# Performance work log

Hardware: AMD Instinct MI355X
Metric: run time of the kernel (lower is better)

## Reference

```python
import jax, jax.numpy as jnp
import numpy as np

B, L, K, T, C_IN, C_OUT, TKS = 32, 1855, 7, 40, 8, 32, 5


def setup_inputs() -> dict:
    key = jax.random.key(0)
    k1, k2, k3, k4 = jax.random.split(key, 4)
    x = jax.random.normal(k1, (B, L, T, C_IN), dtype=jnp.float32)
    idx = jax.random.randint(k2, (L, K), 0, L, dtype=jnp.int32)
    missing = jax.random.uniform(k3, (L, K)) < 0.1
    neighbor_indices = jnp.where(missing, jnp.int32(-1), idx)
    fan_in = K * TKS * C_IN
    fan_out = K * TKS * C_OUT
    limit = np.sqrt(6.0 / (fan_in + fan_out))  # glorot uniform
    kernel = jax.random.uniform(k4, (K, TKS, C_IN, C_OUT), dtype=jnp.float32,
                                minval=-limit, maxval=limit)
    bias = jnp.zeros((C_OUT,), dtype=jnp.float32)
    return {"x": x, "neighbor_indices": neighbor_indices, "kernel": kernel, "bias": bias}


def reference(x, neighbor_indices, kernel, bias):
    # x: (B, L, T, C_in); neighbor_indices: (L, K) with -1 = missing
    mask = (neighbor_indices != -1)
    safe_idx = jnp.where(mask, neighbor_indices, 0)
    # gather neighbor features: (B, L, K, T, C_in)
    nf = x[:, safe_idx]
    nf = nf * mask[None, :, :, None, None].astype(x.dtype)
    tks = kernel.shape[1]
    t_out = x.shape[2] - tks + 1
    # valid temporal conv: sum over small fixed tau instead of materializing
    # the (B, L, K, T_out, tks, C_in) framed tensor
    out = jnp.zeros((x.shape[0], x.shape[1], t_out, kernel.shape[-1]), dtype=x.dtype)
    for tau in range(tks):
        out = out + jnp.einsum('blkti,kio->blto',
                               nf[:, :, :, tau:tau + t_out, :], kernel[:, tau])
    return out + bias
```

## Files before the change

kernel.cpp:

```cpp
#include <hip/hip_runtime.h>

constexpr int Bn = 32, Ln = 1855, Kn = 7, Tn = 40, CIn = 8, COn = 32, TKSn = 5, TOn = 36;
constexpr int BG   = 8;
constexpr int KRED = Kn * TKSn * CIn;
constexpr int KPAD = 288;
constexpr int WROW = 296;
constexpr int XS_ELEMS = BG * Kn * Tn * CIn;
constexpr int XS2 = 4 * Kn * Tn * CIn;
constexpr size_t XN = (size_t)Bn * Ln * Tn * CIn;

constexpr size_t WS_WT   = 0;
constexpr size_t WS_ZPAD = 18432;
constexpr size_t WS_XBF  = 18560;
constexpr size_t WS_NEED = WS_XBF + XN * 2;

typedef __attribute__((ext_vector_type(8))) short bf16x8;
typedef __attribute__((ext_vector_type(8))) unsigned short u16x8;
typedef __attribute__((ext_vector_type(4))) float f32x4;

__device__ inline unsigned short f2bf(float f) {
    unsigned u = __builtin_bit_cast(unsigned, f);
    u += 0x7fffu + ((u >> 16) & 1u);
    return (unsigned short)(u >> 16);
}

__device__ inline void gload_lds16(const void* g, void* lds) {
    __builtin_amdgcn_global_load_lds(
        (const __attribute__((address_space(1))) unsigned int*)g,
        (__attribute__((address_space(3))) unsigned int*)lds,
        16, 0, 0);
}


__global__ __launch_bounds__(256) void prep_w(const float* __restrict__ w,
                                              unsigned short* __restrict__ wt,
                                              unsigned short* __restrict__ zpad) {
    const int tid = threadIdx.x;
    for (int p = tid; p < KRED * COn; p += 256) {
        int o  = p & 31;
        int kr = p >> 5;
        wt[o * KPAD + kr] = f2bf(w[p]);
    }
    for (int p = tid; p < COn * (KPAD - KRED); p += 256) {
        int o = p >> 3;
        wt[o * KPAD + KRED + (p & 7)] = 0;
    }
    if (tid < 64) zpad[tid] = 0;
}

__global__ __launch_bounds__(256) void prep_x(const float* __restrict__ x,
                                              unsigned short* __restrict__ xbf) {
    const size_t n8 = XN / 8;
    for (size_t p = (size_t)blockIdx.x * 256 + threadIdx.x; p < n8;
         p += (size_t)gridDim.x * 256) {
        float4 a = ((const float4*)x)[2 * p];
        float4 b = ((const float4*)x)[2 * p + 1];
        u16x8 v;
        v[0] = f2bf(a.x); v[1] = f2bf(a.y); v[2] = f2bf(a.z); v[3] = f2bf(a.w);
        v[4] = f2bf(b.x); v[5] = f2bf(b.y); v[6] = f2bf(b.z); v[7] = f2bf(b.w);
        *(u16x8*)&xbf[p * 8] = v;
    }
}

__global__ __launch_bounds__(64, 2) void conv_mfma4(
    const unsigned short* __restrict__ xbf,
    const int*   __restrict__ nbr,
    const unsigned short* __restrict__ wt,
    const unsigned short* __restrict__ zpad,
    const float* __restrict__ bias,
    float*       __restrict__ out)
{
    __shared__ unsigned short xs[XS2 + 8];

    const int lane = threadIdx.x;
    const int l    = blockIdx.x;
    const int half = blockIdx.y & 1;
    const int bg   = blockIdx.y >> 1;
    const int b0   = bg * BG + half * 4;

    if (lane < 8) xs[XS2 + lane] = 0;

    int nv = 0;
    if (lane < Kn) nv = nbr[l * Kn + lane];

    #pragma unroll
    for (int s = 0; s < 18; ++s) {
        if (s < 17 || lane < 32) {
            const int u   = s * 64 + lane;
            const int row = u / 40;
            const int q   = u - row * 40;
            const int bl  = row / 7;
            const int k   = row - bl * 7;
            const int l2  = __shfl(nv, k);
            const unsigned short* src = zpad;
            if (l2 >= 0)
                src = xbf + ((size_t)(b0 + bl) * Ln + l2) * 320 + q * 8;
            gload_lds16(src, &xs[s * 512]);
        }
    }

    const int quad = lane >> 4;
    const int lrow = lane & 15;

    bf16x8 bfrag[2][9];
    #pragma unroll
    for (int oh = 0; oh < 2; ++oh)
        #pragma unroll
        for (int c = 0; c < 9; ++c)
            bfrag[oh][c] = *(const bf16x8*)(wt + (oh * 16 + lrow) * KPAD + c * 32 + quad * 8);
    const float bv0 = bias[lrow];
    const float bv1 = bias[16 + lrow];

    asm volatile("s_waitcnt vmcnt(0)" ::: "memory");

    #pragma unroll
    for (int g = 0; g < 3; ++g) {
        const int rt0 = g * 3;
        f32x4 a00 = {0.f,0.f,0.f,0.f};
        f32x4 acc00 = a00, acc01 = a00, acc10 = a00, acc11 = a00, acc20 = a00, acc21 = a00;
        const int m0 = (rt0 + 0) * 16 + lrow;
        const int m1 = (rt0 + 1) * 16 + lrow;
        const int m2 = (rt0 + 2) * 16 + lrow;
        const int bl0 = m0 / 36, t0 = m0 - bl0 * 36;
        const int bl1 = m1 / 36, t1 = m1 - bl1 * 36;
        const int bl2 = m2 / 36, t2 = m2 - bl2 * 36;
        const int base0 = bl0 * 2240 + t0 * 8;
        const int base1 = bl1 * 2240 + t1 * 8;
        const int base2 = bl2 * 2240 + t2 * 8;
        __builtin_amdgcn_s_setprio(1);
        #pragma unroll
        for (int c = 0; c < 9; ++c) {
            const int p = c * 4 + quad;
            const int knbr = p / 5, tau = p - knbr * 5;
            const int koff = knbr * 320 + tau * 8;
            int o0 = base0 + koff, o1 = base1 + koff, o2 = base2 + koff;
            if (c == 8 && quad == 3) { o0 = XS2; o1 = XS2; o2 = XS2; }
            bf16x8 a0 = *(const bf16x8*)&xs[o0];
            bf16x8 a1 = *(const bf16x8*)&xs[o1];
            bf16x8 a2 = *(const bf16x8*)&xs[o2];
            acc00 = __builtin_amdgcn_mfma_f32_16x16x32_bf16(a0, bfrag[0][c], acc00, 0, 0, 0);
            acc01 = __builtin_amdgcn_mfma_f32_16x16x32_bf16(a0, bfrag[1][c], acc01, 0, 0, 0);
            acc10 = __builtin_amdgcn_mfma_f32_16x16x32_bf16(a1, bfrag[0][c], acc10, 0, 0, 0);
            acc11 = __builtin_amdgcn_mfma_f32_16x16x32_bf16(a1, bfrag[1][c], acc11, 0, 0, 0);
            acc20 = __builtin_amdgcn_mfma_f32_16x16x32_bf16(a2, bfrag[0][c], acc20, 0, 0, 0);
            acc21 = __builtin_amdgcn_mfma_f32_16x16x32_bf16(a2, bfrag[1][c], acc21, 0, 0, 0);
        }
        __builtin_amdgcn_s_setprio(0);
        #pragma unroll
        for (int i = 0; i < 3; ++i) {
            const f32x4 c0 = (i == 0) ? acc00 : ((i == 1) ? acc10 : acc20);
            const f32x4 c1 = (i == 0) ? acc01 : ((i == 1) ? acc11 : acc21);
            const int rt = rt0 + i;
            #pragma unroll
            for (int reg = 0; reg < 4; ++reg) {
                const int m  = rt * 16 + quad * 4 + reg;
                const int bl = m / 36, t = m - bl * 36;
                const size_t off =
                    (((size_t)(b0 + bl) * Ln + l) * TOn + t) * COn + lrow;
                __builtin_nontemporal_store(c0[reg] + bv0, &out[off]);
                __builtin_nontemporal_store(c1[reg] + bv1, &out[off + 16]);
            }
        }
    }
}

__global__ __launch_bounds__(256) void conv_mfma(
    const float* __restrict__ x, const int* __restrict__ nbr,
    const float* __restrict__ w, const float* __restrict__ bias,
    float* __restrict__ out)
{
    __shared__ unsigned short xs[XS_ELEMS + 8];
    __shared__ unsigned short wt[COn * WROW];

    const int tid = threadIdx.x;
    const int l   = blockIdx.x;
    const int bg  = blockIdx.y;

    for (int p = tid; p < KRED * COn; p += 256) {
        int o  = p & 31;
        int kr = p >> 5;
        wt[o * WROW + kr] = f2bf(w[p]);
    }
    for (int p = tid; p < COn * (WROW - KRED); p += 256) {
        int o = p >> 4;
        wt[o * WROW + KRED + (p & 15)] = 0;
    }
    if (tid < 8) xs[XS_ELEMS + tid] = 0;

    for (int p = tid; p < BG * Kn * 80; p += 256) {
        int b_local = p / 560;
        int r = p - b_local * 560;
        int k = r / 80;
        int q = r - k * 80;
        int l2 = nbr[l * Kn + k];
        float4 v = make_float4(0.f, 0.f, 0.f, 0.f);
        if (l2 >= 0)
            v = ((const float4*)x)[((size_t)(bg * BG + b_local) * Ln + l2) * 80 + q];
        ushort4 pk;
        pk.x = f2bf(v.x); pk.y = f2bf(v.y); pk.z = f2bf(v.z); pk.w = f2bf(v.w);
        *(ushort4*)&xs[p * 4] = pk;
    }
    __syncthreads();

    const int wave = tid >> 6;
    const int lane = tid & 63;
    const int quad = lane >> 4;
    const int lrow = lane & 15;
    const int o_base  = (wave & 1) * 16;
    const int rt_base = (wave >> 1) * 9;

    bf16x8 bfrag[9];
    #pragma unroll
    for (int c = 0; c < 9; ++c)
        bfrag[c] = *(const bf16x8*)&wt[(o_base + lrow) * WROW + c * 32 + quad * 8];

    const float bv = bias[o_base + lrow];

    #pragma unroll
    for (int g = 0; g < 3; ++g) {
        const int rt0 = rt_base + g * 3;
        f32x4 acc0 = {0.f,0.f,0.f,0.f}, acc1 = acc0, acc2 = acc0;
        const int m0 = (rt0 + 0) * 16 + lrow;
        const int m1 = (rt0 + 1) * 16 + lrow;
        const int m2 = (rt0 + 2) * 16 + lrow;
        const int bl0 = m0 / 36, t0 = m0 - bl0 * 36;
        const int bl1 = m1 / 36, t1 = m1 - bl1 * 36;
        const int bl2 = m2 / 36, t2 = m2 - bl2 * 36;
        const int base0 = bl0 * 2240 + t0 * 8;
        const int base1 = bl1 * 2240 + t1 * 8;
        const int base2 = bl2 * 2240 + t2 * 8;
        #pragma unroll
        for (int c = 0; c < 9; ++c) {
            const int p = c * 4 + quad;
            const int knbr = p / 5, tau = p - knbr * 5;
            const int koff = knbr * 320 + tau * 8;
            int o0 = base0 + koff, o1 = base1 + koff, o2 = base2 + koff;
            if (c == 8 && quad == 3) { o0 = XS_ELEMS; o1 = XS_ELEMS; o2 = XS_ELEMS; }
            bf16x8 a0 = *(const bf16x8*)&xs[o0];
            bf16x8 a1 = *(const bf16x8*)&xs[o1];
            bf16x8 a2 = *(const bf16x8*)&xs[o2];
            acc0 = __builtin_amdgcn_mfma_f32_16x16x32_bf16(a0, bfrag[c], acc0, 0, 0, 0);
            acc1 = __builtin_amdgcn_mfma_f32_16x16x32_bf16(a1, bfrag[c], acc1, 0, 0, 0);
            acc2 = __builtin_amdgcn_mfma_f32_16x16x32_bf16(a2, bfrag[c], acc2, 0, 0, 0);
        }
        #pragma unroll
        for (int i = 0; i < 3; ++i) {
            const f32x4 acc = (i == 0) ? acc0 : ((i == 1) ? acc1 : acc2);
            const int rt = rt0 + i;
            #pragma unroll
            for (int reg = 0; reg < 4; ++reg) {
                const int m  = rt * 16 + quad * 4 + reg;
                const int bl = m / 36, t = m - bl * 36;
                const size_t off =
                    (((size_t)(bg * BG + bl) * Ln + l) * TOn + t) * COn + o_base + lrow;
                out[off] = acc[reg] + bv;
            }
        }
    }
}

extern "C" void kernel_launch(void* const* d_in, const int* in_sizes, int n_in,
                              void* d_out, int out_size, void* d_ws, size_t ws_size,
                              hipStream_t stream) {
    const float* x    = (const float*)d_in[0];
    const int*   nbr  = (const int*)d_in[1];
    const float* w    = (const float*)d_in[2];
    const float* bias = (const float*)d_in[3];
    float*       out  = (float*)d_out;

    if (ws_size >= WS_NEED && d_ws != nullptr) {
        unsigned short* wt   = (unsigned short*)((char*)d_ws + WS_WT);
        unsigned short* zpad = (unsigned short*)((char*)d_ws + WS_ZPAD);
        unsigned short* xbf  = (unsigned short*)((char*)d_ws + WS_XBF);
        prep_w<<<1, 256, 0, stream>>>(w, wt, zpad);
        prep_x<<<2048, 256, 0, stream>>>(x, xbf);
        conv_mfma4<<<dim3(Ln, 8), dim3(64), 0, stream>>>(xbf, nbr, wt, zpad, bias, out);
    } else {
        conv_mfma<<<dim3(Ln, Bn / BG), dim3(256), 0, stream>>>(x, nbr, w, bias, out);
    }
}
```

Baseline: 369.6 us.

## Merge prep kernels and split conv tiles across two waves per block

Folds the weight-prep and x-to-bf16 conversion kernels into a single launch, with one extra block dedicated to weights, which removes one kernel launch. The conv kernel goes from one 64-thread wave per block to two waves that split the gather of the 18 LDS chunks. The two waves then divide the 9 M-tiles 5/4 after a __syncthreads, with launch bounds changed to 128 threads and 4 blocks per CU. The aim is to shorten each block's serial gather and compute path and raise wave-level parallelism, at the cost of a block barrier and an uneven tile split.

```diff
diff --git a/kernel.cpp b/kernel.cpp
--- a/kernel.cpp
+++ b/kernel.cpp
@@ -31,28 +31,27 @@
         16, 0, 0);
 }
 
-
-__global__ __launch_bounds__(256) void prep_w(const float* __restrict__ w,
-                                              unsigned short* __restrict__ wt,
-                                              unsigned short* __restrict__ zpad) {
+__global__ __launch_bounds__(256) void prep_all(const float* __restrict__ x,
+                                                unsigned short* __restrict__ xbf,
+                                                const float* __restrict__ w,
+                                                unsigned short* __restrict__ wt,
+                                                unsigned short* __restrict__ zpad) {
     const int tid = threadIdx.x;
-    for (int p = tid; p < KRED * COn; p += 256) {
-        int o  = p & 31;
-        int kr = p >> 5;
-        wt[o * KPAD + kr] = f2bf(w[p]);
-    }
-    for (int p = tid; p < COn * (KPAD - KRED); p += 256) {
-        int o = p >> 3;
-        wt[o * KPAD + KRED + (p & 7)] = 0;
-    }
-    if (tid < 64) zpad[tid] = 0;
-}
-
-__global__ __launch_bounds__(256) void prep_x(const float* __restrict__ x,
-                                              unsigned short* __restrict__ xbf) {
+    if (blockIdx.x == 2048) {
+        for (int p = tid; p < KRED * COn; p += 256) {
+            int o  = p & 31;
+            int kr = p >> 5;
+            wt[o * KPAD + kr] = f2bf(w[p]);
+        }
+        for (int p = tid; p < COn * (KPAD - KRED); p += 256) {
+            int o = p >> 3;
+            wt[o * KPAD + KRED + (p & 7)] = 0;
+        }
+        if (tid < 64) zpad[tid] = 0;
+        return;
+    }
     const size_t n8 = XN / 8;
-    for (size_t p = (size_t)blockIdx.x * 256 + threadIdx.x; p < n8;
-         p += (size_t)gridDim.x * 256) {
+    for (size_t p = (size_t)blockIdx.x * 256 + tid; p < n8; p += (size_t)2048 * 256) {
         float4 a = ((const float4*)x)[2 * p];
         float4 b = ((const float4*)x)[2 * p + 1];
         u16x8 v;
@@ -62,7 +61,53 @@
     }
 }
 
-__global__ __launch_bounds__(64, 2) void conv_mfma4(
+template<int NT>
+__device__ __forceinline__ void do_tiles(
+    int rt0, const unsigned short* __restrict__ xs,
+    const bf16x8 (&bfrag)[2][9], float bv0, float bv1,
+    float* __restrict__ out, int b0, int l, int quad, int lrow)
+{
+    f32x4 acc[NT][2];
+    int base[NT];
+    #pragma unroll
+    for (int i = 0; i < NT; ++i) {
+        acc[i][0] = f32x4{0.f,0.f,0.f,0.f};
+        acc[i][1] = f32x4{0.f,0.f,0.f,0.f};
+        const int m  = (rt0 + i) * 16 + lrow;
+        const int bl = m / 36, t = m - bl * 36;
+        base[i] = bl * 2240 + t * 8;
+    }
+    __builtin_amdgcn_s_setprio(1);
+    #pragma unroll
+    for (int c = 0; c < 9; ++c) {
+        const int p = c * 4 + quad;
+        const int knbr = p / 5, tau = p - knbr * 5;
+        const int koff = knbr * 320 + tau * 8;
+        #pragma unroll
+        for (int i = 0; i < NT; ++i) {
+            int o = base[i] + koff;
+            if (c == 8 && quad == 3) o = XS2;
+            bf16x8 a = *(const bf16x8*)&xs[o];
+            acc[i][0] = __builtin_amdgcn_mfma_f32_16x16x32_bf16(a, bfrag[0][c], acc[i][0], 0, 0, 0);
+            acc[i][1] = __builtin_amdgcn_mfma_f32_16x16x32_bf16(a, bfrag[1][c], acc[i][1], 0, 0, 0);
+        }
+    }
+    __builtin_amdgcn_s_setprio(0);
+    #pragma unroll
+    for (int i = 0; i < NT; ++i) {
+        #pragma unroll
+        for (int reg = 0; reg < 4; ++reg) {
+            const int m  = (rt0 + i) * 16 + quad * 4 + reg;
+            const int bl = m / 36, t = m - bl * 36;
+            const size_t off =
+                (((size_t)(b0 + bl) * Ln + l) * TOn + t) * COn + lrow;
+            __builtin_nontemporal_store(acc[i][0][reg] + bv0, &out[off]);
+            __builtin_nontemporal_store(acc[i][1][reg] + bv1, &out[off + 16]);
+        }
+    }
+}
+
+__global__ __launch_bounds__(128, 4) void conv_mfma5(
     const unsigned short* __restrict__ xbf,
     const int*   __restrict__ nbr,
     const unsigned short* __restrict__ wt,
@@ -72,21 +117,21 @@
 {
     __shared__ unsigned short xs[XS2 + 8];
 
-    const int lane = threadIdx.x;
+    const int tid  = threadIdx.x;
+    const int wave = tid >> 6;
+    const int lane = tid & 63;
     const int l    = blockIdx.x;
-    const int half = blockIdx.y & 1;
-    const int bg   = blockIdx.y >> 1;
-    const int b0   = bg * BG + half * 4;
-
-    if (lane < 8) xs[XS2 + lane] = 0;
+    const int b0   = blockIdx.y * 4;
+
+    if (tid < 8) xs[XS2 + tid] = 0;
 
     int nv = 0;
     if (lane < Kn) nv = nbr[l * Kn + lane];
 
     #pragma unroll
-    for (int s = 0; s < 18; ++s) {
-        if (s < 17 || lane < 32) {
-            const int u   = s * 64 + lane;
+    for (int ch = wave; ch < 18; ch += 2) {
+        if (ch < 17 || lane < 32) {
+            const int u   = ch * 64 + lane;
             const int row = u / 40;
             const int q   = u - row * 40;
             const int bl  = row / 7;
@@ -95,7 +140,7 @@
             const unsigned short* src = zpad;
             if (l2 >= 0)
                 src = xbf + ((size_t)(b0 + bl) * Ln + l2) * 320 + q * 8;
-            gload_lds16(src, &xs[s * 512]);
+            gload_lds16(src, &xs[ch * 512]);
         }
     }
 
@@ -111,56 +156,14 @@
     const float bv0 = bias[lrow];
     const float bv1 = bias[16 + lrow];
 
-    asm volatile("s_waitcnt vmcnt(0)" ::: "memory");
-
-    #pragma unroll
-    for (int g = 0; g < 3; ++g) {
-        const int rt0 = g * 3;
-        f32x4 a00 = {0.f,0.f,0.f,0.f};
-        f32x4 acc00 = a00, acc01 = a00, acc10 = a00, acc11 = a00, acc20 = a00, acc21 = a00;
-        const int m0 = (rt0 + 0) * 16 + lrow;
-        const int m1 = (rt0 + 1) * 16 + lrow;
-        const int m2 = (rt0 + 2) * 16 + lrow;
-        const int bl0 = m0 / 36, t0 = m0 - bl0 * 36;
-        const int bl1 = m1 / 36, t1 = m1 - bl1 * 36;
-        const int bl2 = m2 / 36, t2 = m2 - bl2 * 36;
-        const int base0 = bl0 * 2240 + t0 * 8;
-        const int base1 = bl1 * 2240 + t1 * 8;
-        const int base2 = bl2 * 2240 + t2 * 8;
-        __builtin_amdgcn_s_setprio(1);
-        #pragma unroll
-        for (int c = 0; c < 9; ++c) {
-            const int p = c * 4 + quad;
-            const int knbr = p / 5, tau = p - knbr * 5;
-            const int koff = knbr * 320 + tau * 8;
-            int o0 = base0 + koff, o1 = base1 + koff, o2 = base2 + koff;
-            if (c == 8 && quad == 3) { o0 = XS2; o1 = XS2; o2 = XS2; }
-            bf16x8 a0 = *(const bf16x8*)&xs[o0];
-            bf16x8 a1 = *(const bf16x8*)&xs[o1];
-            bf16x8 a2 = *(const bf16x8*)&xs[o2];
-            acc00 = __builtin_amdgcn_mfma_f32_16x16x32_bf16(a0, bfrag[0][c], acc00, 0, 0, 0);
-            acc01 = __builtin_amdgcn_mfma_f32_16x16x32_bf16(a0, bfrag[1][c], acc01, 0, 0, 0);
-            acc10 = __builtin_amdgcn_mfma_f32_16x16x32_bf16(a1, bfrag[0][c], acc10, 0, 0, 0);
-            acc11 = __builtin_amdgcn_mfma_f32_16x16x32_bf16(a1, bfrag[1][c], acc11, 0, 0, 0);
-            acc20 = __builtin_amdgcn_mfma_f32_16x16x32_bf16(a2, bfrag[0][c], acc20, 0, 0, 0);
-            acc21 = __builtin_amdgcn_mfma_f32_16x16x32_bf16(a2, bfrag[1][c], acc21, 0, 0, 0);
-        }
-        __builtin_amdgcn_s_setprio(0);
-        #pragma unroll
-        for (int i = 0; i < 3; ++i) {
-            const f32x4 c0 = (i == 0) ? acc00 : ((i == 1) ? acc10 : acc20);
-            const f32x4 c1 = (i == 0) ? acc01 : ((i == 1) ? acc11 : acc21);
-            const int rt = rt0 + i;
-            #pragma unroll
-            for (int reg = 0; reg < 4; ++reg) {
-                const int m  = rt * 16 + quad * 4 + reg;
-                const int bl = m / 36, t = m - bl * 36;
-                const size_t off =
-                    (((size_t)(b0 + bl) * Ln + l) * TOn + t) * COn + lrow;
-                __builtin_nontemporal_store(c0[reg] + bv0, &out[off]);
-                __builtin_nontemporal_store(c1[reg] + bv1, &out[off + 16]);
-            }
-        }
+    __syncthreads();
+
+    if (wave == 0) {
+        do_tiles<3>(0, xs, bfrag, bv0, bv1, out, b0, l, quad, lrow);
+        do_tiles<2>(3, xs, bfrag, bv0, bv1, out, b0, l, quad, lrow);
+    } else {
+        do_tiles<3>(5, xs, bfrag, bv0, bv1, out, b0, l, quad, lrow);
+        do_tiles<1>(8, xs, bfrag, bv0, bv1, out, b0, l, quad, lrow);
     }
 }
 
@@ -272,9 +275,8 @@
         unsigned short* wt   = (unsigned short*)((char*)d_ws + WS_WT);
         unsigned short* zpad = (unsigned short*)((char*)d_ws + WS_ZPAD);
         unsigned short* xbf  = (unsigned short*)((char*)d_ws + WS_XBF);
-        prep_w<<<1, 256, 0, stream>>>(w, wt, zpad);
-        prep_x<<<2048, 256, 0, stream>>>(x, xbf);
-        conv_mfma4<<<dim3(Ln, 8), dim3(64), 0, stream>>>(xbf, nbr, wt, zpad, bias, out);
+        prep_all<<<2049, 256, 0, stream>>>(x, xbf, w, wt, zpad);
+        conv_mfma5<<<dim3(Ln, 8), dim3(128), 0, stream>>>(xbf, nbr, wt, zpad, bias, out);
     } else {
         conv_mfma<<<dim3(Ln, Bn / BG), dim3(256), 0, stream>>>(x, nbr, w, bias, out);
     }
```

Measured after the change: 419.0 us. 1.13x slower.
